# Kernel optimization log

Measured on AMD Instinct MI355X. Metric: run time of the kernel, lower is better.

## Reference

```python
import jax, jax.numpy as jnp
import numpy as np

N_NODES = 50000
N_EDGES = 800000
D = 128
N_LAYERS = 3
N_GRAPHS = 256


def setup_inputs() -> dict:
    key = jax.random.key(0)
    ks = jax.random.split(key, 6)
    x = jax.random.normal(ks[0], (N_NODES, D), dtype=jnp.float32)
    edge_index = jax.random.randint(ks[1], (2, N_EDGES), 0, N_NODES, dtype=jnp.int64)
    batch = jnp.sort(jax.random.randint(ks[2], (N_NODES,), 0, N_GRAPHS, dtype=jnp.int64))
    # Xavier-uniform linear weights (bias filled with 0 per weights_init)
    limit = float(np.sqrt(6.0 / (D + D)))
    W1 = jax.random.uniform(ks[3], (N_LAYERS, D, D), jnp.float32, -limit, limit)
    W2 = jax.random.uniform(ks[4], (N_LAYERS, D, D), jnp.float32, -limit, limit)
    b1 = jnp.zeros((N_LAYERS, D), jnp.float32)
    b2 = jnp.zeros((N_LAYERS, D), jnp.float32)
    return {"x": x, "edge_index": edge_index, "batch": batch,
            "W1": W1, "b1": b1, "W2": W2, "b2": b2}


def reference(x, edge_index, batch, W1, b1, W2, b2):
    src, dst = edge_index[0], edge_index[1]
    h = x  # [N, D]
    pools = []
    for i in range(N_LAYERS):
        # GINConv, eps=0: (1+eps)*h + sum of neighbor (source) features at target
        agg = jax.ops.segment_sum(h[src], dst, num_segments=N_NODES)  # [N, D]
        h = h + agg
        # MLP: Linear -> ReLU -> Linear, then outer ReLU activation
        h = jnp.maximum(h @ W1[i] + b1[i], 0.0) @ W2[i] + b2[i]
        h = jnp.maximum(h, 0.0)
        # global_add_pool over graph ids
        pools.append(jax.ops.segment_sum(h, batch, num_segments=N_GRAPHS))
    return jnp.concatenate(pools, axis=1)  # [N_GRAPHS, N_LAYERS*D]
```

## Files before the change

### kernel.cpp

```cpp
#include <hip/hip_runtime.h>

#define N_NODES 50000
#define N_EDGES 800000
#define DIM 128
#define N_LAYERS 3
#define N_GRAPHS 256
#define OUT_COLS (N_LAYERS * DIM)

#define SUBS 4
#define SUBCAP 24
#define ROWSTRIDE (SUBS * SUBCAP)

typedef __attribute__((ext_vector_type(8))) _Float16 half8;
typedef __attribute__((ext_vector_type(4))) float f32x4;
typedef __attribute__((ext_vector_type(4))) unsigned short us4;
typedef __attribute__((ext_vector_type(8))) short short8;

__global__ void fill_sub_kernel(const int* __restrict__ src, const int* __restrict__ dst,
                                int* __restrict__ deg4, unsigned short* __restrict__ elist) {
    int e = blockIdx.x * blockDim.x + threadIdx.x;
    if (e >= N_EDGES) return;
    int d = dst[e];
    int s = src[e];
    int sub = e & (SUBS - 1);
    int r = atomicAdd(&deg4[d * SUBS + sub], 1);
    if (r < SUBCAP) elist[(size_t)d * ROWSTRIDE + sub * SUBCAP + r] = (unsigned short)s;
}

__global__ void wprep_kernel(const float* __restrict__ W1, const float* __restrict__ W2,
                             _Float16* __restrict__ Wt) {
    int i = blockIdx.x * blockDim.x + threadIdx.x;
    if (i >= 2 * N_LAYERS * DIM * DIM) return;
    int which = i / (N_LAYERS * DIM * DIM);
    int rem = i % (N_LAYERS * DIM * DIM);
    int layer = rem / (DIM * DIM);
    int kj = rem % (DIM * DIM);
    int k = kj / DIM, j = kj % DIM;
    float w = (which ? W2 : W1)[rem];
    int lin = layer * 2 + which;
    Wt[(lin * DIM + j) * DIM + k] = (_Float16)w;
}

__global__ void x2h_kernel(const float* __restrict__ x, unsigned short* __restrict__ x16) {
    int i = blockIdx.x * blockDim.x + threadIdx.x;
    if (i >= N_NODES * DIM / 4) return;
    float4 v = *(const float4*)&x[(size_t)i * 4];
    us4 o;
    _Float16 h0 = (_Float16)v.x, h1 = (_Float16)v.y, h2 = (_Float16)v.z, h3 = (_Float16)v.w;
    o.x = *(unsigned short*)&h0; o.y = *(unsigned short*)&h1;
    o.z = *(unsigned short*)&h2; o.w = *(unsigned short*)&h3;
    *(us4*)&x16[(size_t)i * 4] = o;
}

__global__ __launch_bounds__(256) void gather_kernel(
        const unsigned short* __restrict__ hin, const int* __restrict__ deg4,
        const unsigned short* __restrict__ elist,
        unsigned short* __restrict__ agg_hi, unsigned short* __restrict__ agg_lo) {
    int node = (blockIdx.x * blockDim.x + threadIdx.x) >> 5;
    int lane = threadIdx.x & 31;
    if (node >= N_NODES) return;
    union H4 { uint2 u; _Float16 h[4]; };
    const size_t rb = (size_t)node * DIM + lane * 4;
    H4 s;
    s.u = *(const uint2*)&hin[rb];
    float a0 = (float)s.h[0], a1 = (float)s.h[1], a2 = (float)s.h[2], a3 = (float)s.h[3];
    int4 c4 = *(const int4*)&deg4[node * SUBS];
#pragma unroll
    for (int sub = 0; sub < SUBS; sub++) {
        int cnt = ((const int*)&c4)[sub];
        if (cnt > SUBCAP) cnt = SUBCAP;
        const unsigned short* el = &elist[(size_t)node * ROWSTRIDE + sub * SUBCAP];
        int i = 0;
        for (; i + 4 <= cnt; i += 4) {
            int e0 = el[i], e1 = el[i + 1], e2 = el[i + 2], e3 = el[i + 3];
            H4 v0, v1, v2, v3;
            v0.u = *(const uint2*)&hin[(size_t)e0 * DIM + lane * 4];
            v1.u = *(const uint2*)&hin[(size_t)e1 * DIM + lane * 4];
            v2.u = *(const uint2*)&hin[(size_t)e2 * DIM + lane * 4];
            v3.u = *(const uint2*)&hin[(size_t)e3 * DIM + lane * 4];
            a0 += ((float)v0.h[0] + (float)v1.h[0]) + ((float)v2.h[0] + (float)v3.h[0]);
            a1 += ((float)v0.h[1] + (float)v1.h[1]) + ((float)v2.h[1] + (float)v3.h[1]);
            a2 += ((float)v0.h[2] + (float)v1.h[2]) + ((float)v2.h[2] + (float)v3.h[2]);
            a3 += ((float)v0.h[3] + (float)v1.h[3]) + ((float)v2.h[3] + (float)v3.h[3]);
        }
        for (; i < cnt; i++) {
            H4 v0;
            v0.u = *(const uint2*)&hin[(size_t)el[i] * DIM + lane * 4];
            a0 += (float)v0.h[0];
            a1 += (float)v0.h[1];
            a2 += (float)v0.h[2];
            a3 += (float)v0.h[3];
        }
    }
    float av[4] = {a0, a1, a2, a3};
    unsigned short hb[4], lb[4];
#pragma unroll
    for (int j = 0; j < 4; j++) {
        _Float16 hi = (_Float16)av[j];
        _Float16 lo = (_Float16)(av[j] - (float)hi);
        hb[j] = *(unsigned short*)&hi;
        lb[j] = *(unsigned short*)&lo;
    }
    uint2 oh, ol;
    oh.x = (unsigned)hb[0] | ((unsigned)hb[1] << 16);
    oh.y = (unsigned)hb[2] | ((unsigned)hb[3] << 16);
    ol.x = (unsigned)lb[0] | ((unsigned)lb[1] << 16);
    ol.y = (unsigned)lb[2] | ((unsigned)lb[3] << 16);
    *(uint2*)&agg_hi[rb] = oh;
    *(uint2*)&agg_lo[rb] = ol;
}

__global__ __launch_bounds__(64, 4) void mlp_pool_wave_kernel(
        const unsigned short* __restrict__ Ahi, const unsigned short* __restrict__ Alo,
        const _Float16* __restrict__ Wt,
        const float* __restrict__ bias1, const float* __restrict__ bias2,
        const int* __restrict__ batch, unsigned short* __restrict__ h16out,
        float* __restrict__ pool_out, int layer, int write_h) {
    __shared__ float S[16][132];
    __shared__ int gb[16];
    const int l = threadIdx.x;
    const int lr = l & 15;
    const int lk = l >> 4;
    const int row0 = blockIdx.x * 16;

    if (l < 16) gb[l] = batch[row0 + l];

    const size_t ab = (size_t)(row0 + lr) * DIM + lk * 8;
    half8 ah[4], al[4];
#pragma unroll
    for (int kb = 0; kb < 4; kb++) {
        ah[kb] = *(const half8*)&Ahi[ab + kb * 32];
        al[kb] = *(const half8*)&Alo[ab + kb * 32];
    }

#pragma unroll
    for (int cb = 0; cb < 8; cb++) {
        const _Float16* wp = &Wt[(cb * 16 + lr) * DIM + lk * 8];
        half8 w[4];
#pragma unroll
        for (int kb = 0; kb < 4; kb++) w[kb] = *(const half8*)&wp[kb * 32];
        f32x4 aA = {0.f, 0.f, 0.f, 0.f}, aC = aA;
#pragma unroll
        for (int kb = 0; kb < 4; kb++) {
            aA = __builtin_amdgcn_mfma_f32_16x16x32_f16(ah[kb], w[kb], aA, 0, 0, 0);
            aC = __builtin_amdgcn_mfma_f32_16x16x32_f16(al[kb], w[kb], aC, 0, 0, 0);
        }
        float bv = bias1[cb * 16 + lr];
#pragma unroll
        for (int r = 0; r < 4; r++)
            S[lk * 4 + r][cb * 16 + lr] = fmaxf(aA[r] + aC[r] + bv, 0.f);
    }

    half8 ch[4], cl[4];
#pragma unroll
    for (int kb = 0; kb < 4; kb++) {
        const float* sr = &S[lr][kb * 32 + lk * 8];
        f32x4 u0 = *(const f32x4*)&sr[0];
        f32x4 u1 = *(const f32x4*)&sr[4];
        float uu[8] = {u0.x, u0.y, u0.z, u0.w, u1.x, u1.y, u1.z, u1.w};
        half8 hh, ll;
#pragma unroll
        for (int j = 0; j < 8; j++) {
            _Float16 hv = (_Float16)uu[j];
            hh[j] = hv;
            ll[j] = (_Float16)(uu[j] - (float)hv);
        }
        ch[kb] = hh;
        cl[kb] = ll;
    }

    const _Float16* W2 = Wt + DIM * DIM;
#pragma unroll
    for (int cb = 0; cb < 8; cb++) {
        const _Float16* wp = &W2[(cb * 16 + lr) * DIM + lk * 8];
        half8 w[4];
#pragma unroll
        for (int kb = 0; kb < 4; kb++) w[kb] = *(const half8*)&wp[kb * 32];
        f32x4 aA = {0.f, 0.f, 0.f, 0.f}, aC = aA;
#pragma unroll
        for (int kb = 0; kb < 4; kb++) {
            aA = __builtin_amdgcn_mfma_f32_16x16x32_f16(ch[kb], w[kb], aA, 0, 0, 0);
            aC = __builtin_amdgcn_mfma_f32_16x16x32_f16(cl[kb], w[kb], aC, 0, 0, 0);
        }
        float bv = bias2[cb * 16 + lr];
#pragma unroll
        for (int r = 0; r < 4; r++)
            S[lk * 4 + r][cb * 16 + lr] = fmaxf(aA[r] + aC[r] + bv, 0.f);
    }

    if (write_h) {
        const int r = l >> 2, c0 = (l & 3) * 32;
        unsigned short buf[32];
#pragma unroll
        for (int j = 0; j < 32; j++) {
            _Float16 hv = (_Float16)S[r][c0 + j];
            buf[j] = *(unsigned short*)&hv;
        }
        const size_t ob = (size_t)(row0 + r) * DIM + c0;
#pragma unroll
        for (int q = 0; q < 4; q++)
            *(short8*)&h16out[ob + q * 8] = *(const short8*)&buf[q * 8];
    }

    const int d0 = 2 * l;
    float p0 = 0.f, p1 = 0.f;
    int curg = gb[0];
    for (int r = 0; r < 16; r++) {
        int g = gb[r];
        if (g != curg) {
            atomicAdd(&pool_out[curg * OUT_COLS + layer * DIM + d0], p0);
            atomicAdd(&pool_out[curg * OUT_COLS + layer * DIM + d0 + 1], p1);
            p0 = p1 = 0.f;
            curg = g;
        }
        p0 += S[r][d0];
        p1 += S[r][d0 + 1];
    }
    atomicAdd(&pool_out[curg * OUT_COLS + layer * DIM + d0], p0);
    atomicAdd(&pool_out[curg * OUT_COLS + layer * DIM + d0 + 1], p1);
}


extern "C" void kernel_launch(void* const* d_in, const int* in_sizes, int n_in,
                              void* d_out, int out_size, void* d_ws, size_t ws_size,
                              hipStream_t stream) {
    const float* x = (const float*)d_in[0];
    const int* ei = (const int*)d_in[1];
    const int* batch = (const int*)d_in[2];
    const float* W1 = (const float*)d_in[3];
    const float* b1 = (const float*)d_in[4];
    const float* W2 = (const float*)d_in[5];
    const float* b2 = (const float*)d_in[6];
    float* out = (float*)d_out;

    const int* src = ei;
    const int* dst = ei + N_EDGES;

    char* ws = (char*)d_ws;
    unsigned short* buf0 = (unsigned short*)ws;
    unsigned short* agg_hi = (unsigned short*)(ws + 12800000);
    unsigned short* agg_lo = (unsigned short*)(ws + 25600000);
    int* deg4 = (int*)(ws + 38400000);
    _Float16* Wt = (_Float16*)(ws + 39200000);
    unsigned short* elist = (unsigned short*)(ws + 39396608);

    hipMemsetAsync(d_out, 0, (size_t)out_size * sizeof(float), stream);
    hipMemsetAsync(deg4, 0, (size_t)N_NODES * SUBS * sizeof(int), stream);

    fill_sub_kernel<<<(N_EDGES + 255) / 256, 256, 0, stream>>>(src, dst, deg4, elist);

    x2h_kernel<<<(N_NODES * DIM / 4 + 255) / 256, 256, 0, stream>>>(x, buf0);

    wprep_kernel<<<(2 * N_LAYERS * DIM * DIM + 255) / 256, 256, 0, stream>>>(W1, W2, Wt);

    const int gather_grid = (N_NODES * 32 + 255) / 256;
    const int mlp_grid = N_NODES / 16;

    for (int layer = 0; layer < N_LAYERS; layer++) {
        gather_kernel<<<gather_grid, 256, 0, stream>>>(buf0, deg4, elist, agg_hi, agg_lo);
        mlp_pool_wave_kernel<<<mlp_grid, 64, 0, stream>>>(
            agg_hi, agg_lo, Wt + (size_t)layer * 2 * DIM * DIM,
            b1 + layer * DIM, b2 + layer * DIM, batch, buf0, out, layer,
            (layer < N_LAYERS - 1) ? 1 : 0);
    }
}
```

Baseline: 290.3 us.

## Drop fp16 hi/lo split for aggregates and merge prep kernels into one

The gather kernel now stores the aggregated sum as a single fp16 value instead of a hi/lo fp16 pair. This halves aggregate write and read traffic and halves the first-layer MFMA count in the MLP kernel. Separately, the edge-list fill, x-to-fp16 conversion and weight transpose kernels are merged into one launch, with block ranges assigned to each task, which cuts launch overhead. The cost is lower precision in the first linear layer's input, since sums of about 16 neighbours can lose accuracy in fp16.

```diff
diff --git a/kernel.cpp b/kernel.cpp
--- a/kernel.cpp
+++ b/kernel.cpp
@@ -11,51 +11,54 @@
 #define SUBCAP 24
 #define ROWSTRIDE (SUBS * SUBCAP)
 
+#define FILL_NB 3125
+#define X2H_NB 6250
+#define WPREP_NB 384
+
 typedef __attribute__((ext_vector_type(8))) _Float16 half8;
 typedef __attribute__((ext_vector_type(4))) float f32x4;
 typedef __attribute__((ext_vector_type(4))) unsigned short us4;
 typedef __attribute__((ext_vector_type(8))) short short8;
 
-__global__ void fill_sub_kernel(const int* __restrict__ src, const int* __restrict__ dst,
-                                int* __restrict__ deg4, unsigned short* __restrict__ elist) {
-    int e = blockIdx.x * blockDim.x + threadIdx.x;
-    if (e >= N_EDGES) return;
-    int d = dst[e];
-    int s = src[e];
-    int sub = e & (SUBS - 1);
-    int r = atomicAdd(&deg4[d * SUBS + sub], 1);
-    if (r < SUBCAP) elist[(size_t)d * ROWSTRIDE + sub * SUBCAP + r] = (unsigned short)s;
-}
-
-__global__ void wprep_kernel(const float* __restrict__ W1, const float* __restrict__ W2,
-                             _Float16* __restrict__ Wt) {
-    int i = blockIdx.x * blockDim.x + threadIdx.x;
-    if (i >= 2 * N_LAYERS * DIM * DIM) return;
-    int which = i / (N_LAYERS * DIM * DIM);
-    int rem = i % (N_LAYERS * DIM * DIM);
-    int layer = rem / (DIM * DIM);
-    int kj = rem % (DIM * DIM);
-    int k = kj / DIM, j = kj % DIM;
-    float w = (which ? W2 : W1)[rem];
-    int lin = layer * 2 + which;
-    Wt[(lin * DIM + j) * DIM + k] = (_Float16)w;
-}
-
-__global__ void x2h_kernel(const float* __restrict__ x, unsigned short* __restrict__ x16) {
-    int i = blockIdx.x * blockDim.x + threadIdx.x;
-    if (i >= N_NODES * DIM / 4) return;
-    float4 v = *(const float4*)&x[(size_t)i * 4];
-    us4 o;
-    _Float16 h0 = (_Float16)v.x, h1 = (_Float16)v.y, h2 = (_Float16)v.z, h3 = (_Float16)v.w;
-    o.x = *(unsigned short*)&h0; o.y = *(unsigned short*)&h1;
-    o.z = *(unsigned short*)&h2; o.w = *(unsigned short*)&h3;
-    *(us4*)&x16[(size_t)i * 4] = o;
+__global__ __launch_bounds__(256) void prep_kernel(
+        const int* __restrict__ src, const int* __restrict__ dst,
+        int* __restrict__ deg4, unsigned short* __restrict__ elist,
+        const float* __restrict__ x, unsigned short* __restrict__ x16,
+        const float* __restrict__ W1, const float* __restrict__ W2,
+        _Float16* __restrict__ Wt) {
+    const int b = blockIdx.x;
+    if (b < FILL_NB) {
+        int e = b * 256 + threadIdx.x;
+        int d = dst[e];
+        int s = src[e];
+        int sub = e & (SUBS - 1);
+        int r = atomicAdd(&deg4[d * SUBS + sub], 1);
+        if (r < SUBCAP) elist[(size_t)d * ROWSTRIDE + sub * SUBCAP + r] = (unsigned short)s;
+    } else if (b < FILL_NB + X2H_NB) {
+        int i = (b - FILL_NB) * 256 + threadIdx.x;
+        float4 v = *(const float4*)&x[(size_t)i * 4];
+        us4 o;
+        _Float16 h0 = (_Float16)v.x, h1 = (_Float16)v.y, h2 = (_Float16)v.z, h3 = (_Float16)v.w;
+        o.x = *(unsigned short*)&h0; o.y = *(unsigned short*)&h1;
+        o.z = *(unsigned short*)&h2; o.w = *(unsigned short*)&h3;
+        *(us4*)&x16[(size_t)i * 4] = o;
+    } else {
+        int i = (b - FILL_NB - X2H_NB) * 256 + threadIdx.x;
+        int which = i / (N_LAYERS * DIM * DIM);
+        int rem = i % (N_LAYERS * DIM * DIM);
+        int layer = rem / (DIM * DIM);
+        int kj = rem % (DIM * DIM);
+        int k = kj / DIM, j = kj % DIM;
+        float w = (which ? W2 : W1)[rem];
+        int lin = layer * 2 + which;
+        Wt[(lin * DIM + j) * DIM + k] = (_Float16)w;
+    }
 }
 
 __global__ __launch_bounds__(256) void gather_kernel(
         const unsigned short* __restrict__ hin, const int* __restrict__ deg4,
         const unsigned short* __restrict__ elist,
-        unsigned short* __restrict__ agg_hi, unsigned short* __restrict__ agg_lo) {
+        unsigned short* __restrict__ agg) {
     int node = (blockIdx.x * blockDim.x + threadIdx.x) >> 5;
     int lane = threadIdx.x & 31;
     if (node >= N_NODES) return;
@@ -92,26 +95,15 @@
             a3 += (float)v0.h[3];
         }
     }
-    float av[4] = {a0, a1, a2, a3};
-    unsigned short hb[4], lb[4];
-#pragma unroll
-    for (int j = 0; j < 4; j++) {
-        _Float16 hi = (_Float16)av[j];
-        _Float16 lo = (_Float16)(av[j] - (float)hi);
-        hb[j] = *(unsigned short*)&hi;
-        lb[j] = *(unsigned short*)&lo;
-    }
-    uint2 oh, ol;
-    oh.x = (unsigned)hb[0] | ((unsigned)hb[1] << 16);
-    oh.y = (unsigned)hb[2] | ((unsigned)hb[3] << 16);
-    ol.x = (unsigned)lb[0] | ((unsigned)lb[1] << 16);
-    ol.y = (unsigned)lb[2] | ((unsigned)lb[3] << 16);
-    *(uint2*)&agg_hi[rb] = oh;
-    *(uint2*)&agg_lo[rb] = ol;
+    _Float16 h0 = (_Float16)a0, h1 = (_Float16)a1, h2 = (_Float16)a2, h3 = (_Float16)a3;
+    uint2 oh;
+    oh.x = (unsigned)*(unsigned short*)&h0 | ((unsigned)*(unsigned short*)&h1 << 16);
+    oh.y = (unsigned)*(unsigned short*)&h2 | ((unsigned)*(unsigned short*)&h3 << 16);
+    *(uint2*)&agg[rb] = oh;
 }
 
 __global__ __launch_bounds__(64, 4) void mlp_pool_wave_kernel(
-        const unsigned short* __restrict__ Ahi, const unsigned short* __restrict__ Alo,
+        const unsigned short* __restrict__ Agg,
         const _Float16* __restrict__ Wt,
         const float* __restrict__ bias1, const float* __restrict__ bias2,
         const int* __restrict__ batch, unsigned short* __restrict__ h16out,
@@ -126,12 +118,9 @@
     if (l < 16) gb[l] = batch[row0 + l];
 
     const size_t ab = (size_t)(row0 + lr) * DIM + lk * 8;
-    half8 ah[4], al[4];
-#pragma unroll
-    for (int kb = 0; kb < 4; kb++) {
-        ah[kb] = *(const half8*)&Ahi[ab + kb * 32];
-        al[kb] = *(const half8*)&Alo[ab + kb * 32];
-    }
+    half8 ah[4];
+#pragma unroll
+    for (int kb = 0; kb < 4; kb++) ah[kb] = *(const half8*)&Agg[ab + kb * 32];
 
 #pragma unroll
     for (int cb = 0; cb < 8; cb++) {
@@ -139,16 +128,14 @@
         half8 w[4];
 #pragma unroll
         for (int kb = 0; kb < 4; kb++) w[kb] = *(const half8*)&wp[kb * 32];
-        f32x4 aA = {0.f, 0.f, 0.f, 0.f}, aC = aA;
-#pragma unroll
-        for (int kb = 0; kb < 4; kb++) {
+        f32x4 aA = {0.f, 0.f, 0.f, 0.f};
+#pragma unroll
+        for (int kb = 0; kb < 4; kb++)
             aA = __builtin_amdgcn_mfma_f32_16x16x32_f16(ah[kb], w[kb], aA, 0, 0, 0);
-            aC = __builtin_amdgcn_mfma_f32_16x16x32_f16(al[kb], w[kb], aC, 0, 0, 0);
-        }
         float bv = bias1[cb * 16 + lr];
 #pragma unroll
         for (int r = 0; r < 4; r++)
-            S[lk * 4 + r][cb * 16 + lr] = fmaxf(aA[r] + aC[r] + bv, 0.f);
+            S[lk * 4 + r][cb * 16 + lr] = fmaxf(aA[r] + bv, 0.f);
     }
 
     half8 ch[4], cl[4];
@@ -238,28 +225,24 @@
 
     char* ws = (char*)d_ws;
     unsigned short* buf0 = (unsigned short*)ws;
-    unsigned short* agg_hi = (unsigned short*)(ws + 12800000);
-    unsigned short* agg_lo = (unsigned short*)(ws + 25600000);
-    int* deg4 = (int*)(ws + 38400000);
-    _Float16* Wt = (_Float16*)(ws + 39200000);
-    unsigned short* elist = (unsigned short*)(ws + 39396608);
+    unsigned short* agg = (unsigned short*)(ws + 12800000);
+    int* deg4 = (int*)(ws + 25600000);
+    _Float16* Wt = (_Float16*)(ws + 26400000);
+    unsigned short* elist = (unsigned short*)(ws + 26596608);
 
     hipMemsetAsync(d_out, 0, (size_t)out_size * sizeof(float), stream);
     hipMemsetAsync(deg4, 0, (size_t)N_NODES * SUBS * sizeof(int), stream);
 
-    fill_sub_kernel<<<(N_EDGES + 255) / 256, 256, 0, stream>>>(src, dst, deg4, elist);
-
-    x2h_kernel<<<(N_NODES * DIM / 4 + 255) / 256, 256, 0, stream>>>(x, buf0);
-
-    wprep_kernel<<<(2 * N_LAYERS * DIM * DIM + 255) / 256, 256, 0, stream>>>(W1, W2, Wt);
+    prep_kernel<<<FILL_NB + X2H_NB + WPREP_NB, 256, 0, stream>>>(
+        src, dst, deg4, elist, x, buf0, W1, W2, Wt);
 
     const int gather_grid = (N_NODES * 32 + 255) / 256;
     const int mlp_grid = N_NODES / 16;
 
     for (int layer = 0; layer < N_LAYERS; layer++) {
-        gather_kernel<<<gather_grid, 256, 0, stream>>>(buf0, deg4, elist, agg_hi, agg_lo);
+        gather_kernel<<<gather_grid, 256, 0, stream>>>(buf0, deg4, elist, agg);
         mlp_pool_wave_kernel<<<mlp_grid, 64, 0, stream>>>(
-            agg_hi, agg_lo, Wt + (size_t)layer * 2 * DIM * DIM,
+            agg, Wt + (size_t)layer * 2 * DIM * DIM,
             b1 + layer * DIM, b2 + layer * DIM, batch, buf0, out, layer,
             (layer < N_LAYERS - 1) ? 1 : 0);
     }
```

New measurement: 284.2 us. 2.1% less time.
